# Kernel tuning notes

Measured on AMD Instinct MI355X. Metric: run time of the kernel, lower is better.

The kernel has to match this reference:

```python
import jax, jax.numpy as jnp
import numpy as np

LEAKY_SLOPE = 0.2   # LeakyReLU alpha from __init__
MASK_VAL = -9.0e15  # same sentinel as torch reference


def setup_inputs() -> dict:
    key = jax.random.key(0)
    k1, k2, k3 = jax.random.split(key, 3)
    B, N, D = 512, 64, 128
    hidden = jax.random.normal(k1, (B, N, D), dtype=jnp.float32)
    adj = jax.random.randint(k2, (B, N, N), 0, 5)  # edge types 0..4
    a = jax.random.normal(k3, (4, D), dtype=jnp.float32) * 0.1  # stacked a_0..a_3
    return {"hidden": hidden, "adj": adj, "a": a}


def reference(hidden, adj, a):
    # e_k[b,i,j] = leakyrelu( sum_d hidden[b,i,d]*hidden[b,j,d]*a[k,d] )
    # Never materializes the [B,N,N,D] tensor: contract (hidden * a_k) @ hidden^T.
    e = jnp.einsum('kd,bid,bjd->kbij', a, hidden, hidden)  # [4,B,N,N]
    e = jnp.where(e >= 0, e, LEAKY_SLOPE * e)
    mask = jnp.full(e.shape[1:], MASK_VAL, dtype=e.dtype)
    alpha = jnp.where(adj == 1, e[0], mask)
    alpha = jnp.where(adj == 2, e[1], alpha)
    alpha = jnp.where(adj == 3, e[2], alpha)
    alpha = jnp.where(adj == 4, e[3], alpha)
    alpha = jax.nn.softmax(alpha, axis=-1)          # [B,N,N]
    return jnp.matmul(alpha, hidden)                # [B,N,D]
```

## Files before the change

kernel.cpp:

```cpp
#include <hip/hip_runtime.h>
#include <hip/hip_bf16.h>


#define NB 512
#define NN 64
#define ND 128
#define HS 136
#define AS 72

typedef __bf16 bf16x8 __attribute__((ext_vector_type(8)));
typedef __bf16 bf16x4 __attribute__((ext_vector_type(4)));
typedef float  f32x4  __attribute__((ext_vector_type(4)));

__global__ __launch_bounds__(256)
void gat_kernel(const float* __restrict__ hidden,
                const int*   __restrict__ adj,
                const float* __restrict__ a,
                float*       __restrict__ out)
{
    __shared__ __bf16 h_lds[NN * HS];
    __shared__ __bf16 h_tr[8 * NN * 16];
    __shared__ __bf16 al_lds[NN * AS];
    __shared__ float  a_lds[4 * ND];

    const int t = threadIdx.x;
    const int l = t & 63;
    const int w = t >> 6;
    const int b = blockIdx.x;
    const int g  = l >> 4;
    const int g8 = g << 3;
    const int i0 = w * 16 + (g << 2);

    const float4* hin = (const float4*)(hidden + (size_t)b * NN * ND);
    float4 sv[8];
    int srow[8], sc4[8];
    #pragma unroll
    for (int s = 0; s < 8; ++s) {
        srow[s] = ((l >> 2) & 15) | ((s >> 1) << 4);
        int f4  = (l & 3) | (w << 2) | ((s & 1) << 4);
        sc4[s]  = f4 << 2;
        sv[s] = hin[srow[s] * 32 + f4];
    }
    const float av0 = a[t];
    const float av1 = a[t + 256];

    #pragma unroll
    for (int s = 0; s < 8; ++s) {
        float4 v = sv[s];
        bf16x4 pk = { (__bf16)v.x, (__bf16)v.y, (__bf16)v.z, (__bf16)v.w };
        *(bf16x4*)&h_lds[srow[s] * HS + sc4[s]] = pk;
        *(bf16x4*)&h_tr[((sc4[s] >> 4) << 10) + (srow[s] << 4) + (sc4[s] & 15)] = pk;
    }
    a_lds[t]       = av0;
    a_lds[t + 256] = av1;
    __syncthreads();

    const int* adjb = adj + (size_t)b * NN * NN;
    int adjv[4][4];
    #pragma unroll
    for (int ct = 0; ct < 4; ++ct)
        #pragma unroll
        for (int r = 0; r < 4; ++r)
            adjv[ct][r] = adjb[(i0 + r) * NN + ct * 16 + (l & 15)];

    const int irow = w * 16 + (l & 15);
    f32x4 acc[4][4];
    #pragma unroll
    for (int ct = 0; ct < 4; ++ct)
        #pragma unroll
        for (int k = 0; k < 4; ++k)
            acc[ct][k] = (f32x4){0.f, 0.f, 0.f, 0.f};

    #pragma unroll
    for (int kk = 0; kk < 4; ++kk) {
        int d0 = kk * 32 + g8;
        bf16x8 hf = *(const bf16x8*)&h_lds[irow * HS + d0];
        float hff[8];
        #pragma unroll
        for (int e = 0; e < 8; ++e) hff[e] = (float)hf[e];
        bf16x8 hk[4];
        #pragma unroll
        for (int k = 0; k < 4; ++k) {
            float4 alo = *(const float4*)&a_lds[k * ND + d0];
            float4 ahi = *(const float4*)&a_lds[k * ND + d0 + 4];
            bf16x8 r;
            r[0] = (__bf16)(hff[0] * alo.x); r[1] = (__bf16)(hff[1] * alo.y);
            r[2] = (__bf16)(hff[2] * alo.z); r[3] = (__bf16)(hff[3] * alo.w);
            r[4] = (__bf16)(hff[4] * ahi.x); r[5] = (__bf16)(hff[5] * ahi.y);
            r[6] = (__bf16)(hff[6] * ahi.z); r[7] = (__bf16)(hff[7] * ahi.w);
            hk[k] = r;
        }
        bf16x8 bfr[4];
        #pragma unroll
        for (int ct = 0; ct < 4; ++ct)
            bfr[ct] = *(const bf16x8*)&h_lds[(ct * 16 + (l & 15)) * HS + d0];
        __builtin_amdgcn_s_setprio(1);
        #pragma unroll
        for (int ct = 0; ct < 4; ++ct)
            #pragma unroll
            for (int k = 0; k < 4; ++k)
                acc[ct][k] = __builtin_amdgcn_mfma_f32_16x16x32_bf16(hk[k], bfr[ct], acc[ct][k], 0, 0, 0);
        __builtin_amdgcn_s_setprio(0);
    }

    #pragma unroll
    for (int ct = 0; ct < 4; ++ct)
        #pragma unroll
        for (int r = 0; r < 4; ++r) {
            int av = adjv[ct][r];
            float v = av == 1 ? acc[ct][0][r]
                    : av == 2 ? acc[ct][1][r]
                    : av == 3 ? acc[ct][2][r]
                    : av == 4 ? acc[ct][3][r] : -9.0e15f;
            v = fmaxf(v, 0.2f * v);
            float p = __expf(v);
            al_lds[(i0 + r) * AS + ct * 16 + (l & 15)] = (__bf16)p;
        }

    const int ia = w * 16 + (l & 15);
    bf16x8 aA0 = *(const bf16x8*)&al_lds[ia * AS + g8];
    bf16x8 aA1 = *(const bf16x8*)&al_lds[ia * AS + 32 + g8];
    bf16x8 ones;
    #pragma unroll
    for (int e = 0; e < 8; ++e) ones[e] = (__bf16)1.0f;
    f32x4 sacc = {0.f, 0.f, 0.f, 0.f};
    sacc = __builtin_amdgcn_mfma_f32_16x16x32_bf16(aA0, ones, sacc, 0, 0, 0);
    sacc = __builtin_amdgcn_mfma_f32_16x16x32_bf16(aA1, ones, sacc, 0, 0, 0);
    float inv[4];
    #pragma unroll
    for (int r = 0; r < 4; ++r) inv[r] = __builtin_amdgcn_rcpf(sacc[r]);

    unsigned trb = (unsigned)(unsigned long long)(&h_tr[0])
                 + (unsigned)(((l & 15) << 3) + (g << 8));
    bf16x4 tr[8][4];
#define TRR(dst, off) asm volatile("ds_read_b64_tr_b16 %0, %1 offset:" #off : "=v"(dst) : "v"(trb));
    TRR(tr[0][0], 0)     TRR(tr[0][1], 128)   TRR(tr[0][2], 1024)  TRR(tr[0][3], 1152)
    TRR(tr[1][0], 2048)  TRR(tr[1][1], 2176)  TRR(tr[1][2], 3072)  TRR(tr[1][3], 3200)
    TRR(tr[2][0], 4096)  TRR(tr[2][1], 4224)  TRR(tr[2][2], 5120)  TRR(tr[2][3], 5248)
    TRR(tr[3][0], 6144)  TRR(tr[3][1], 6272)  TRR(tr[3][2], 7168)  TRR(tr[3][3], 7296)
    TRR(tr[4][0], 8192)  TRR(tr[4][1], 8320)  TRR(tr[4][2], 9216)  TRR(tr[4][3], 9344)
    TRR(tr[5][0], 10240) TRR(tr[5][1], 10368) TRR(tr[5][2], 11264) TRR(tr[5][3], 11392)
    TRR(tr[6][0], 12288) TRR(tr[6][1], 12416) TRR(tr[6][2], 13312) TRR(tr[6][3], 13440)
    TRR(tr[7][0], 14336) TRR(tr[7][1], 14464) TRR(tr[7][2], 15360) TRR(tr[7][3], 15488)
#undef TRR
    asm volatile("s_waitcnt lgkmcnt(0)" ::: "memory");
    __builtin_amdgcn_sched_barrier(0);

    float* outb = out + (size_t)b * NN * ND;
    #pragma unroll
    for (int dt = 0; dt < 8; ++dt) {
        bf16x8 B0 = __builtin_shufflevector(tr[dt][0], tr[dt][1], 0, 1, 2, 3, 4, 5, 6, 7);
        bf16x8 B1 = __builtin_shufflevector(tr[dt][2], tr[dt][3], 0, 1, 2, 3, 4, 5, 6, 7);
        __builtin_amdgcn_s_setprio(1);
        f32x4 o = {0.f, 0.f, 0.f, 0.f};
        o = __builtin_amdgcn_mfma_f32_16x16x32_bf16(aA0, B0, o, 0, 0, 0);
        o = __builtin_amdgcn_mfma_f32_16x16x32_bf16(aA1, B1, o, 0, 0, 0);
        __builtin_amdgcn_s_setprio(0);
        int dr = dt * 16 + (l & 15);
        #pragma unroll
        for (int r = 0; r < 4; ++r)
            outb[(i0 + r) * ND + dr] = o[r] * inv[r];
    }
}

extern "C" void kernel_launch(void* const* d_in, const int* in_sizes, int n_in,
                              void* d_out, int out_size, void* d_ws, size_t ws_size,
                              hipStream_t stream) {
    const float* hidden = (const float*)d_in[0];
    const int*   adj    = (const int*)d_in[1];
    const float* a      = (const float*)d_in[2];
    float*       out    = (float*)d_out;
    gat_kernel<<<NB, 256, 0, stream>>>(hidden, adj, a, out);
}
```

Before: 14.87 us.

## Use 128-thread blocks with two row tiles per wave and alias the alpha buffer

Halves the block size so each wave computes 32 output rows (two 16-row tiles) instead of 16. The B-fragments of hidden are then loaded once and reused across both row tiles. The alpha buffer now reuses the hidden LDS area after a new barrier, cutting shared memory per block. The transpose reads are issued before the exp and softmax stage so their latency can overlap it. In exchange, per-wave register use roughly doubles and there are half as many waves per block to hide latency.

```diff
diff --git a/kernel.cpp b/kernel.cpp
--- a/kernel.cpp
+++ b/kernel.cpp
@@ -12,7 +12,7 @@
 typedef __bf16 bf16x4 __attribute__((ext_vector_type(4)));
 typedef float  f32x4  __attribute__((ext_vector_type(4)));
 
-__global__ __launch_bounds__(256)
+__global__ __launch_bounds__(128, 2)
 void gat_kernel(const float* __restrict__ hidden,
                 const int*   __restrict__ adj,
                 const float* __restrict__ a,
@@ -20,8 +20,8 @@
 {
     __shared__ __bf16 h_lds[NN * HS];
     __shared__ __bf16 h_tr[8 * NN * 16];
-    __shared__ __bf16 al_lds[NN * AS];
     __shared__ float  a_lds[4 * ND];
+    __bf16* al_lds = h_lds;
 
     const int t = threadIdx.x;
     const int l = t & 63;
@@ -29,66 +29,69 @@
     const int b = blockIdx.x;
     const int g  = l >> 4;
     const int g8 = g << 3;
-    const int i0 = w * 16 + (g << 2);
 
     const float4* hin = (const float4*)(hidden + (size_t)b * NN * ND);
-    float4 sv[8];
-    int srow[8], sc4[8];
+    float4 sv[16];
+    int srow[16], sc4[16];
     #pragma unroll
-    for (int s = 0; s < 8; ++s) {
-        srow[s] = ((l >> 2) & 15) | ((s >> 1) << 4);
-        int f4  = (l & 3) | (w << 2) | ((s & 1) << 4);
+    for (int s = 0; s < 16; ++s) {
+        srow[s] = ((l >> 2) & 15) | ((s >> 2) << 4);
+        int f4  = (l & 3) | (w << 2) | ((s & 3) << 3);
         sc4[s]  = f4 << 2;
         sv[s] = hin[srow[s] * 32 + f4];
     }
-    const float av0 = a[t];
-    const float av1 = a[t + 256];
+    const float av0 = a[t], av1 = a[t + 128], av2 = a[t + 256], av3 = a[t + 384];
 
     #pragma unroll
-    for (int s = 0; s < 8; ++s) {
+    for (int s = 0; s < 16; ++s) {
         float4 v = sv[s];
         bf16x4 pk = { (__bf16)v.x, (__bf16)v.y, (__bf16)v.z, (__bf16)v.w };
         *(bf16x4*)&h_lds[srow[s] * HS + sc4[s]] = pk;
         *(bf16x4*)&h_tr[((sc4[s] >> 4) << 10) + (srow[s] << 4) + (sc4[s] & 15)] = pk;
     }
-    a_lds[t]       = av0;
-    a_lds[t + 256] = av1;
+    a_lds[t] = av0; a_lds[t + 128] = av1; a_lds[t + 256] = av2; a_lds[t + 384] = av3;
     __syncthreads();
 
     const int* adjb = adj + (size_t)b * NN * NN;
-    int adjv[4][4];
+    int adjv[2][4][4];
     #pragma unroll
-    for (int ct = 0; ct < 4; ++ct)
+    for (int rt = 0; rt < 2; ++rt)
         #pragma unroll
-        for (int r = 0; r < 4; ++r)
-            adjv[ct][r] = adjb[(i0 + r) * NN + ct * 16 + (l & 15)];
+        for (int ct = 0; ct < 4; ++ct)
+            #pragma unroll
+            for (int r = 0; r < 4; ++r)
+                adjv[rt][ct][r] = adjb[(w * 32 + rt * 16 + g * 4 + r) * NN + ct * 16 + (l & 15)];
 
-    const int irow = w * 16 + (l & 15);
-    f32x4 acc[4][4];
+    f32x4 acc[2][4][4];
     #pragma unroll
-    for (int ct = 0; ct < 4; ++ct)
+    for (int rt = 0; rt < 2; ++rt)
         #pragma unroll
-        for (int k = 0; k < 4; ++k)
-            acc[ct][k] = (f32x4){0.f, 0.f, 0.f, 0.f};
+        for (int ct = 0; ct < 4; ++ct)
+            #pragma unroll
+            for (int k = 0; k < 4; ++k)
+                acc[rt][ct][k] = (f32x4){0.f, 0.f, 0.f, 0.f};
 
     #pragma unroll
     for (int kk = 0; kk < 4; ++kk) {
         int d0 = kk * 32 + g8;
-        bf16x8 hf = *(const bf16x8*)&h_lds[irow * HS + d0];
-        float hff[8];
+        bf16x8 hk[2][4];
         #pragma unroll
-        for (int e = 0; e < 8; ++e) hff[e] = (float)hf[e];
-        bf16x8 hk[4];
-        #pragma unroll
-        for (int k = 0; k < 4; ++k) {
-            float4 alo = *(const float4*)&a_lds[k * ND + d0];
-            float4 ahi = *(const float4*)&a_lds[k * ND + d0 + 4];
-            bf16x8 r;
-            r[0] = (__bf16)(hff[0] * alo.x); r[1] = (__bf16)(hff[1] * alo.y);
-            r[2] = (__bf16)(hff[2] * alo.z); r[3] = (__bf16)(hff[3] * alo.w);
-            r[4] = (__bf16)(hff[4] * ahi.x); r[5] = (__bf16)(hff[5] * ahi.y);
-            r[6] = (__bf16)(hff[6] * ahi.z); r[7] = (__bf16)(hff[7] * ahi.w);
-            hk[k] = r;
+        for (int rt = 0; rt < 2; ++rt) {
+            bf16x8 hf = *(const bf16x8*)&h_lds[(w * 32 + rt * 16 + (l & 15)) * HS + d0];
+            float hff[8];
+            #pragma unroll
+            for (int e = 0; e < 8; ++e) hff[e] = (float)hf[e];
+            #pragma unroll
+            for (int k = 0; k < 4; ++k) {
+                float4 alo = *(const float4*)&a_lds[k * ND + d0];
+                float4 ahi = *(const float4*)&a_lds[k * ND + d0 + 4];
+                bf16x8 r;
+                r[0] = (__bf16)(hff[0] * alo.x); r[1] = (__bf16)(hff[1] * alo.y);
+                r[2] = (__bf16)(hff[2] * alo.z); r[3] = (__bf16)(hff[3] * alo.w);
+                r[4] = (__bf16)(hff[4] * ahi.x); r[5] = (__bf16)(hff[5] * ahi.y);
+                r[6] = (__bf16)(hff[6] * ahi.z); r[7] = (__bf16)(hff[7] * ahi.w);
+                hk[rt][k] = r;
+            }
         }
         bf16x8 bfr[4];
         #pragma unroll
@@ -96,39 +99,15 @@
             bfr[ct] = *(const bf16x8*)&h_lds[(ct * 16 + (l & 15)) * HS + d0];
         __builtin_amdgcn_s_setprio(1);
         #pragma unroll
-        for (int ct = 0; ct < 4; ++ct)
+        for (int rt = 0; rt < 2; ++rt)
             #pragma unroll
-            for (int k = 0; k < 4; ++k)
-                acc[ct][k] = __builtin_amdgcn_mfma_f32_16x16x32_bf16(hk[k], bfr[ct], acc[ct][k], 0, 0, 0);
+            for (int ct = 0; ct < 4; ++ct)
+                #pragma unroll
+                for (int k = 0; k < 4; ++k)
+                    acc[rt][ct][k] = __builtin_amdgcn_mfma_f32_16x16x32_bf16(hk[rt][k], bfr[ct], acc[rt][ct][k], 0, 0, 0);
         __builtin_amdgcn_s_setprio(0);
     }
-
-    #pragma unroll
-    for (int ct = 0; ct < 4; ++ct)
-        #pragma unroll
-        for (int r = 0; r < 4; ++r) {
-            int av = adjv[ct][r];
-            float v = av == 1 ? acc[ct][0][r]
-                    : av == 2 ? acc[ct][1][r]
-                    : av == 3 ? acc[ct][2][r]
-                    : av == 4 ? acc[ct][3][r] : -9.0e15f;
-            v = fmaxf(v, 0.2f * v);
-            float p = __expf(v);
-            al_lds[(i0 + r) * AS + ct * 16 + (l & 15)] = (__bf16)p;
-        }
-
-    const int ia = w * 16 + (l & 15);
-    bf16x8 aA0 = *(const bf16x8*)&al_lds[ia * AS + g8];
-    bf16x8 aA1 = *(const bf16x8*)&al_lds[ia * AS + 32 + g8];
-    bf16x8 ones;
-    #pragma unroll
-    for (int e = 0; e < 8; ++e) ones[e] = (__bf16)1.0f;
-    f32x4 sacc = {0.f, 0.f, 0.f, 0.f};
-    sacc = __builtin_amdgcn_mfma_f32_16x16x32_bf16(aA0, ones, sacc, 0, 0, 0);
-    sacc = __builtin_amdgcn_mfma_f32_16x16x32_bf16(aA1, ones, sacc, 0, 0, 0);
-    float inv[4];
-    #pragma unroll
-    for (int r = 0; r < 4; ++r) inv[r] = __builtin_amdgcn_rcpf(sacc[r]);
+    __syncthreads();
 
     unsigned trb = (unsigned)(unsigned long long)(&h_tr[0])
                  + (unsigned)(((l & 15) << 3) + (g << 8));
@@ -143,6 +122,40 @@
     TRR(tr[6][0], 12288) TRR(tr[6][1], 12416) TRR(tr[6][2], 13312) TRR(tr[6][3], 13440)
     TRR(tr[7][0], 14336) TRR(tr[7][1], 14464) TRR(tr[7][2], 15360) TRR(tr[7][3], 15488)
 #undef TRR
+
+    #pragma unroll
+    for (int rt = 0; rt < 2; ++rt)
+        #pragma unroll
+        for (int ct = 0; ct < 4; ++ct)
+            #pragma unroll
+            for (int r = 0; r < 4; ++r) {
+                int av = adjv[rt][ct][r];
+                float v = av == 1 ? acc[rt][ct][0][r]
+                        : av == 2 ? acc[rt][ct][1][r]
+                        : av == 3 ? acc[rt][ct][2][r]
+                        : av == 4 ? acc[rt][ct][3][r] : -9.0e15f;
+                v = fmaxf(v, 0.2f * v);
+                float p = __expf(v);
+                al_lds[(w * 32 + rt * 16 + g * 4 + r) * AS + ct * 16 + (l & 15)] = (__bf16)p;
+            }
+
+    bf16x8 ones;
+    #pragma unroll
+    for (int e = 0; e < 8; ++e) ones[e] = (__bf16)1.0f;
+    bf16x8 aA0[2], aA1[2];
+    float inv[2][4];
+    #pragma unroll
+    for (int rt = 0; rt < 2; ++rt) {
+        int ia = w * 32 + rt * 16 + (l & 15);
+        aA0[rt] = *(const bf16x8*)&al_lds[ia * AS + g8];
+        aA1[rt] = *(const bf16x8*)&al_lds[ia * AS + 32 + g8];
+        f32x4 sacc = {0.f, 0.f, 0.f, 0.f};
+        sacc = __builtin_amdgcn_mfma_f32_16x16x32_bf16(aA0[rt], ones, sacc, 0, 0, 0);
+        sacc = __builtin_amdgcn_mfma_f32_16x16x32_bf16(aA1[rt], ones, sacc, 0, 0, 0);
+        #pragma unroll
+        for (int r = 0; r < 4; ++r) inv[rt][r] = __builtin_amdgcn_rcpf(sacc[r]);
+    }
+
     asm volatile("s_waitcnt lgkmcnt(0)" ::: "memory");
     __builtin_amdgcn_sched_barrier(0);
 
@@ -151,15 +164,18 @@
     for (int dt = 0; dt < 8; ++dt) {
         bf16x8 B0 = __builtin_shufflevector(tr[dt][0], tr[dt][1], 0, 1, 2, 3, 4, 5, 6, 7);
         bf16x8 B1 = __builtin_shufflevector(tr[dt][2], tr[dt][3], 0, 1, 2, 3, 4, 5, 6, 7);
-        __builtin_amdgcn_s_setprio(1);
-        f32x4 o = {0.f, 0.f, 0.f, 0.f};
-        o = __builtin_amdgcn_mfma_f32_16x16x32_bf16(aA0, B0, o, 0, 0, 0);
-        o = __builtin_amdgcn_mfma_f32_16x16x32_bf16(aA1, B1, o, 0, 0, 0);
-        __builtin_amdgcn_s_setprio(0);
         int dr = dt * 16 + (l & 15);
         #pragma unroll
-        for (int r = 0; r < 4; ++r)
-            outb[(i0 + r) * ND + dr] = o[r] * inv[r];
+        for (int rt = 0; rt < 2; ++rt) {
+            __builtin_amdgcn_s_setprio(1);
+            f32x4 o = {0.f, 0.f, 0.f, 0.f};
+            o = __builtin_amdgcn_mfma_f32_16x16x32_bf16(aA0[rt], B0, o, 0, 0, 0);
+            o = __builtin_amdgcn_mfma_f32_16x16x32_bf16(aA1[rt], B1, o, 0, 0, 0);
+            __builtin_amdgcn_s_setprio(0);
+            #pragma unroll
+            for (int r = 0; r < 4; ++r)
+                outb[(w * 32 + rt * 16 + g * 4 + r) * ND + dr] = o[r] * inv[rt][r];
+        }
     }
 }
 
@@ -170,5 +186,5 @@
     const int*   adj    = (const int*)d_in[1];
     const float* a      = (const float*)d_in[2];
     float*       out    = (float*)d_out;
-    gat_kernel<<<NB, 256, 0, stream>>>(hidden, adj, a, out);
+    gat_kernel<<<NB, 128, 0, stream>>>(hidden, adj, a, out);
 }
```

Measured after the change: 19.38 us. +30.4%, slower.
